# Performance work log

Hardware: AMD Instinct MI355X
Metric: run time of the kernel (lower is better)

Reference implementation:

```python
import jax, jax.numpy as jnp
import numpy as np

B, S, D, H = 4, 2048, 1024, 16
HD = D // H  # head dim = 64
EPS = 1e-12


def setup_inputs() -> dict:
    key = jax.random.key(0)
    ks = jax.random.split(key, 9)
    sc = 1.0 / np.sqrt(D)
    return {
        "X": jax.random.normal(ks[0], (B, S, D), jnp.float32),
        "Wq": jax.random.normal(ks[1], (D, D), jnp.float32) * sc,
        "bq": jnp.zeros((D,), jnp.float32),
        "Wk": jax.random.normal(ks[2], (D, D), jnp.float32) * sc,
        "bk": jnp.zeros((D,), jnp.float32),
        "Wv": jax.random.normal(ks[3], (D, D), jnp.float32) * sc,
        "bv": jnp.zeros((D,), jnp.float32),
        "Wo": jax.random.normal(ks[4], (D, D), jnp.float32) * sc,
        "bo": jnp.zeros((D,), jnp.float32),
        "gamma": jnp.ones((D,), jnp.float32),
        "beta": jnp.zeros((D,), jnp.float32),
    }


def _attention_block(X, Wq, bq, Wk, bk, Wv, bv, Wo, bo, gamma, beta):
    def heads(t):  # [B,S,D] -> [B,H,S,HD]
        return t.reshape(B, S, H, HD).transpose(0, 2, 1, 3)

    Q = heads(X @ Wq.T + bq)
    K = heads(X @ Wk.T + bk)
    V = heads(X @ Wv.T + bv)
    A = jnp.einsum("bhqd,bhkd->bhqk", Q, K) / np.sqrt(HD)
    A = jax.nn.softmax(A, axis=-1)
    O = jnp.einsum("bhqk,bhkd->bhqd", A, V)
    O = O.transpose(0, 2, 1, 3).reshape(B, S, D)
    O = O @ Wo.T + bo
    Y = O + X
    mu = Y.mean(-1, keepdims=True)
    var = jnp.square(Y - mu).mean(-1, keepdims=True)
    return gamma * (Y - mu) / jnp.sqrt(var + EPS) + beta


def reference(X, Wq, bq, Wk, bk, Wv, bv, Wo, bo, gamma, beta):
    return _attention_block(X, Wq, bq, Wk, bk, Wv, bv, Wo, bo, gamma, beta)
```

## Files before the change

### kernel.cpp

```cpp
#include <hip/hip_runtime.h>
#include <hip/hip_bf16.h>

#define B_ 4
#define S_ 2048
#define D_ 1024
#define H_ 16
#define HD_ 64
#define M_ (B_*S_)
#define BH_ (B_*H_)

typedef __bf16 bf16;
typedef __attribute__((ext_vector_type(8))) __bf16 bf16x8;
typedef __attribute__((ext_vector_type(4))) __bf16 bf16x4;
typedef __attribute__((ext_vector_type(4))) float f32x4;

#define MFMA16(a,b,c) __builtin_amdgcn_mfma_f32_16x16x32_bf16((a),(b),(c),0,0,0)

__device__ __forceinline__ void gl2lds16(const void* g, void* l) {
  __builtin_amdgcn_global_load_lds(
      (__attribute__((address_space(1))) void*)(g),
      (__attribute__((address_space(3))) void*)(l), 16, 0, 0);
}

__device__ __forceinline__ float fexp2(float x) {
  float r;
  asm("v_exp_f32 %0, %1" : "=v"(r) : "v"(x));
  return r;
}

__global__ __launch_bounds__(256) void k_cvt(const float* __restrict__ in,
                                             bf16* __restrict__ out, int n) {
  int i = (blockIdx.x * 256 + threadIdx.x) * 4;
  if (i >= n) return;
  f32x4 v = *(const f32x4*)(in + i);
  bf16x4 o;
  o[0] = (bf16)v[0]; o[1] = (bf16)v[1]; o[2] = (bf16)v[2]; o[3] = (bf16)v[3];
  *(bf16x4*)(out + i) = o;
}

template <int EPI>
__global__ __launch_bounds__(512, 4) void k_gemm(const bf16* __restrict__ A,
                                                 const bf16* __restrict__ W,
                                                 const float* __restrict__ bias,
                                                 const float* __restrict__ Xres,
                                                 void* __restrict__ outp,
                                                 float scale) {
  __shared__ __align__(16) bf16 As[2][128 * 64];
  __shared__ __align__(16) bf16 Bs[2][128 * 64];
  const int t = threadIdx.x;
  const int l = t & 63, w = t >> 6;
  const int g = l >> 4, c = l & 15;
  const int wm = w >> 2, wn = w & 3;
  const int m0 = blockIdx.y * 128, n0 = blockIdx.x * 128;

  f32x4 acc[4][2];
#pragma unroll
  for (int i = 0; i < 4; ++i)
#pragma unroll
    for (int j = 0; j < 2; ++j) acc[i][j] = (f32x4)(0.0f);

  const int srow = t >> 3;
  const int schk = t & 7;

#define STG(buf, k0)                                                          \
  do {                                                                        \
    for (int p = 0; p < 2; ++p) {                                             \
      const int row = p * 64 + srow;                                          \
      const int sc = (schk ^ (row & 7)) * 8;                                  \
      gl2lds16(A + (size_t)(m0 + row) * D_ + (k0) + sc,                       \
               &As[buf][p * 4096 + t * 8]);                                   \
      gl2lds16(W + (size_t)(n0 + row) * D_ + (k0) + sc,                       \
               &Bs[buf][p * 4096 + t * 8]);                                   \
    }                                                                         \
  } while (0)

  STG(0, 0);
  __syncthreads();

  for (int kt = 0; kt < D_ / 64; ++kt) {
    const int cur = kt & 1;
    if (kt + 1 < D_ / 64) STG(cur ^ 1, (kt + 1) * 64);
#pragma unroll
    for (int kk = 0; kk < 2; ++kk) {
      bf16x8 af[4], bw[2];
#pragma unroll
      for (int i = 0; i < 4; ++i) {
        const int ra = wm * 64 + i * 16 + c;
        af[i] = *(const bf16x8*)&As[cur][ra * 64 + (((kk * 4 + g) ^ (ra & 7)) * 8)];
      }
#pragma unroll
      for (int j = 0; j < 2; ++j) {
        const int rb = wn * 32 + j * 16 + c;
        bw[j] = *(const bf16x8*)&Bs[cur][rb * 64 + (((kk * 4 + g) ^ (rb & 7)) * 8)];
      }
#pragma unroll
      for (int i = 0; i < 4; ++i)
#pragma unroll
        for (int j = 0; j < 2; ++j) acc[i][j] = MFMA16(af[i], bw[j], acc[i][j]);
    }
    __syncthreads();
  }
#undef STG

  float bv[2];
#pragma unroll
  for (int j = 0; j < 2; ++j) bv[j] = bias[n0 + wn * 32 + j * 16 + c];

#pragma unroll
  for (int i = 0; i < 4; ++i) {
#pragma unroll
    for (int j = 0; j < 2; ++j) {
#pragma unroll
      for (int r = 0; r < 4; ++r) {
        const int m = m0 + wm * 64 + i * 16 + g * 4 + r;
        const int n = n0 + wn * 32 + j * 16 + c;
        const float v = (acc[i][j][r] + bv[j]) * scale;
        if (EPI == 2) {
          ((float*)outp)[(size_t)m * D_ + n] = v + Xres[(size_t)m * D_ + n];
        } else {
          const int b = m >> 11, s = m & (S_ - 1);
          const int h = n >> 6, hd = n & 63;
          size_t idx;
          if (EPI == 0) idx = (((size_t)(b * H_ + h)) * S_ + s) * HD_ + hd;
          else          idx = (((size_t)(b * H_ + h)) * HD_ + hd) * S_ + s;
          ((bf16*)outp)[idx] = (bf16)v;
        }
      }
    }
  }
}

__global__ __launch_bounds__(512, 4) void k_attn(const bf16* __restrict__ Q,
                                                 const bf16* __restrict__ K,
                                                 const bf16* __restrict__ Vt,
                                                 bf16* __restrict__ O) {
  __shared__ __align__(16) bf16 Ks[2][64 * 64];
  __shared__ __align__(16) bf16 Vs[2][64 * 64];
  __shared__ __align__(16) bf16 Pl[8][16 * 72];
  const int t = threadIdx.x;
  const int l = t & 63, w = t >> 6;
  const int g = l >> 4, c = l & 15;
  const int bh = blockIdx.y;
  const int q0 = blockIdx.x * 256 + w * 32;
  const bf16* Qh = Q + (size_t)bh * S_ * HD_;
  const bf16* Kh = K + (size_t)bh * S_ * HD_;
  const bf16* Vh = Vt + (size_t)bh * HD_ * S_;

  bf16x8 qf[2][2];
#pragma unroll
  for (int mf = 0; mf < 2; ++mf)
#pragma unroll
    for (int kk = 0; kk < 2; ++kk)
      qf[mf][kk] = *(const bf16x8*)&Qh[(size_t)(q0 + mf * 16 + c) * HD_ + kk * 32 + g * 8];

  f32x4 acc[2][4];
  float m_c[2], l_c[2];
#pragma unroll
  for (int mf = 0; mf < 2; ++mf) {
#pragma unroll
    for (int nf = 0; nf < 4; ++nf) acc[mf][nf] = (f32x4)(0.0f);
    m_c[mf] = -__builtin_inff();
    l_c[mf] = 0.f;
  }

  const int srow = t >> 3, schk = t & 7;

#define STGA(buf, kt)                                                         \
  do {                                                                        \
    const int sck = (schk ^ (srow & 7)) * 8;                                  \
    gl2lds16(Kh + (size_t)((kt) * 64 + srow) * HD_ + sck, &Ks[buf][t * 8]);   \
    gl2lds16(Vh + (size_t)srow * S_ + (kt) * 64 + sck, &Vs[buf][t * 8]);      \
  } while (0)

  STGA(0, 0);
  __syncthreads();

  for (int kt = 0; kt < S_ / 64; ++kt) {
    const int cur = kt & 1;
    if (kt + 1 < S_ / 64) STGA(cur ^ 1, kt + 1);

    f32x4 st[2][4];
#pragma unroll
    for (int mf = 0; mf < 2; ++mf)
#pragma unroll
      for (int nf = 0; nf < 4; ++nf) st[mf][nf] = (f32x4)(0.0f);

#pragma unroll
    for (int kk = 0; kk < 2; ++kk) {
      bf16x8 kf[4];
#pragma unroll
      for (int nf = 0; nf < 4; ++nf) {
        const int rw = nf * 16 + c;
        kf[nf] = *(const bf16x8*)&Ks[cur][rw * 64 + (((kk * 4 + g) ^ (rw & 7)) * 8)];
      }
#pragma unroll
      for (int mf = 0; mf < 2; ++mf)
#pragma unroll
        for (int nf = 0; nf < 4; ++nf)
          st[mf][nf] = MFMA16(kf[nf], qf[mf][kk], st[mf][nf]);
    }

#pragma unroll
    for (int mf = 0; mf < 2; ++mf) {
      float tm = st[mf][0][0];
#pragma unroll
      for (int nf = 0; nf < 4; ++nf)
#pragma unroll
        for (int r = 0; r < 4; ++r)
          if (nf || r) tm = fmaxf(tm, st[mf][nf][r]);
      tm = fmaxf(tm, __shfl_xor(tm, 16));
      tm = fmaxf(tm, __shfl_xor(tm, 32));
      const float mn = fmaxf(m_c[mf], tm);
      const float cfq = fexp2(m_c[mf] - mn);
      m_c[mf] = mn;
      float rs = 0.f;
#pragma unroll
      for (int nf = 0; nf < 4; ++nf) {
        bf16x4 pv;
#pragma unroll
        for (int r = 0; r < 4; ++r) {
          const float p = fexp2(st[mf][nf][r] - mn);
          rs += p;
          pv[r] = (bf16)p;
        }
        *(bf16x4*)&Pl[w][c * 72 + nf * 16 + 4 * g] = pv;
      }
      rs += __shfl_xor(rs, 16);
      rs += __shfl_xor(rs, 32);
      l_c[mf] = l_c[mf] * cfq + rs;

      float cfr[4];
#pragma unroll
      for (int r = 0; r < 4; ++r) cfr[r] = __shfl(cfq, 4 * g + r);
#pragma unroll
      for (int nf = 0; nf < 4; ++nf)
#pragma unroll
        for (int r = 0; r < 4; ++r) acc[mf][nf][r] *= cfr[r];

#pragma unroll
      for (int kk = 0; kk < 2; ++kk) {
        bf16x8 pa = *(const bf16x8*)&Pl[w][c * 72 + kk * 32 + g * 8];
        bf16x8 vf[4];
#pragma unroll
        for (int nf = 0; nf < 4; ++nf) {
          const int rw = nf * 16 + c;
          vf[nf] = *(const bf16x8*)&Vs[cur][rw * 64 + (((kk * 4 + g) ^ (rw & 7)) * 8)];
        }
#pragma unroll
        for (int nf = 0; nf < 4; ++nf)
          acc[mf][nf] = MFMA16(pa, vf[nf], acc[mf][nf]);
      }
    }
    __syncthreads();
  }
#undef STGA

  const int b = bh >> 4, h = bh & 15;
#pragma unroll
  for (int mf = 0; mf < 2; ++mf) {
    float li[4];
#pragma unroll
    for (int r = 0; r < 4; ++r)
      li[r] = __builtin_amdgcn_rcpf(__shfl(l_c[mf], 4 * g + r));
#pragma unroll
    for (int nf = 0; nf < 4; ++nf)
#pragma unroll
      for (int r = 0; r < 4; ++r) {
        const int q = q0 + mf * 16 + 4 * g + r;
        const int dv = nf * 16 + c;
        O[((size_t)(b * S_ + q)) * D_ + h * 64 + dv] = (bf16)(acc[mf][nf][r] * li[r]);
      }
  }
}

__global__ __launch_bounds__(256) void k_ln(const float* __restrict__ Y,
                                            const float* __restrict__ gamma,
                                            const float* __restrict__ beta,
                                            float* __restrict__ out) {
  __shared__ float red[8];
  const int row = blockIdx.x, t = threadIdx.x;
  const float* y = Y + (size_t)row * D_;
  f32x4 v = *(const f32x4*)(y + t * 4);
  float s = v[0] + v[1] + v[2] + v[3];
  float s2 = v[0]*v[0] + v[1]*v[1] + v[2]*v[2] + v[3]*v[3];
#pragma unroll
  for (int mk = 1; mk <= 32; mk <<= 1) {
    s += __shfl_xor(s, mk);
    s2 += __shfl_xor(s2, mk);
  }
  if ((t & 63) == 0) { red[t >> 6] = s; red[4 + (t >> 6)] = s2; }
  __syncthreads();
  const float ts = red[0] + red[1] + red[2] + red[3];
  const float ts2 = red[4] + red[5] + red[6] + red[7];
  const float mu = ts * (1.0f / D_);
  const float inv = rsqrtf(ts2 * (1.0f / D_) - mu * mu + 1e-12f);
  f32x4 gm = *(const f32x4*)(gamma + t * 4);
  f32x4 bt = *(const f32x4*)(beta + t * 4);
  f32x4 o;
#pragma unroll
  for (int j = 0; j < 4; ++j) o[j] = gm[j] * (v[j] - mu) * inv + bt[j];
  *(f32x4*)(out + (size_t)row * D_ + t * 4) = o;
}

extern "C" void kernel_launch(void* const* d_in, const int* in_sizes, int n_in,
                              void* d_out, int out_size, void* d_ws, size_t ws_size,
                              hipStream_t stream) {
  const float* X     = (const float*)d_in[0];
  const float* Wq    = (const float*)d_in[1];
  const float* bq    = (const float*)d_in[2];
  const float* Wk    = (const float*)d_in[3];
  const float* bk    = (const float*)d_in[4];
  const float* Wv    = (const float*)d_in[5];
  const float* bv    = (const float*)d_in[6];
  const float* Wo    = (const float*)d_in[7];
  const float* bo    = (const float*)d_in[8];
  const float* gamma = (const float*)d_in[9];
  const float* beta  = (const float*)d_in[10];

  char* ws = (char*)d_ws;
  bf16* Xb  = (bf16*)(ws + 0);
  bf16* Wqb = (bf16*)(ws + (16u << 20));
  bf16* Wkb = (bf16*)(ws + (18u << 20));
  bf16* Wvb = (bf16*)(ws + (20u << 20));
  bf16* Wob = (bf16*)(ws + (22u << 20));
  bf16* Qb  = (bf16*)(ws + (24u << 20));
  bf16* Kb  = (bf16*)(ws + (40u << 20));
  bf16* Vt  = (bf16*)(ws + (56u << 20));
  bf16* Ob  = (bf16*)(ws + (72u << 20));
  float* Yb = (float*)(ws + (88u << 20));

  const float SCL = 0.125f * 1.44269504088896340736f;

  k_cvt<<<M_ * D_ / 1024, 256, 0, stream>>>(X, Xb, M_ * D_);
  k_cvt<<<D_ * D_ / 1024, 256, 0, stream>>>(Wq, Wqb, D_ * D_);
  k_cvt<<<D_ * D_ / 1024, 256, 0, stream>>>(Wk, Wkb, D_ * D_);
  k_cvt<<<D_ * D_ / 1024, 256, 0, stream>>>(Wv, Wvb, D_ * D_);
  k_cvt<<<D_ * D_ / 1024, 256, 0, stream>>>(Wo, Wob, D_ * D_);

  dim3 gg(D_ / 128, M_ / 128);
  k_gemm<0><<<gg, 512, 0, stream>>>(Xb, Wqb, bq, nullptr, Qb, SCL);
  k_gemm<0><<<gg, 512, 0, stream>>>(Xb, Wkb, bk, nullptr, Kb, 1.0f);
  k_gemm<1><<<gg, 512, 0, stream>>>(Xb, Wvb, bv, nullptr, Vt, 1.0f);
  k_attn<<<dim3(S_ / 256, BH_), 512, 0, stream>>>(Qb, Kb, Vt, Ob);
  k_gemm<2><<<gg, 512, 0, stream>>>(Ob, Wob, bo, X, Yb, 1.0f);
  k_ln<<<M_, 256, 0, stream>>>(Yb, gamma, beta, (float*)d_out);
}
```

Before: 335.2 us.

## Rewrite attention inner loop with 32x32 MFMA and register-resident P

```diff
diff --git a/kernel.cpp b/kernel.cpp
--- a/kernel.cpp
+++ b/kernel.cpp
@@ -13,8 +13,11 @@
 typedef __attribute__((ext_vector_type(8))) __bf16 bf16x8;
 typedef __attribute__((ext_vector_type(4))) __bf16 bf16x4;
 typedef __attribute__((ext_vector_type(4))) float f32x4;
+typedef __attribute__((ext_vector_type(16))) float f32x16;
+typedef __attribute__((ext_vector_type(4))) unsigned u32x4;
 
 #define MFMA16(a,b,c) __builtin_amdgcn_mfma_f32_16x16x32_bf16((a),(b),(c),0,0,0)
+#define MFMA32(a,b,c) __builtin_amdgcn_mfma_f32_32x32x16_bf16((a),(b),(c),0,0,0)
 
 __device__ __forceinline__ void gl2lds16(const void* g, void* l) {
   __builtin_amdgcn_global_load_lds(
@@ -25,6 +28,12 @@
 __device__ __forceinline__ float fexp2(float x) {
   float r;
   asm("v_exp_f32 %0, %1" : "=v"(r) : "v"(x));
+  return r;
+}
+
+__device__ __forceinline__ unsigned cvtpk(float lo, float hi) {
+  unsigned r;
+  asm("v_cvt_pk_bf16_f32 %0, %1, %2" : "=v"(r) : "v"(lo), "v"(hi));
   return r;
 }
 
@@ -130,46 +139,42 @@
   }
 }
 
-__global__ __launch_bounds__(512, 4) void k_attn(const bf16* __restrict__ Q,
+__global__ __launch_bounds__(256, 3) void k_attn(const bf16* __restrict__ Q,
                                                  const bf16* __restrict__ K,
                                                  const bf16* __restrict__ Vt,
                                                  bf16* __restrict__ O) {
   __shared__ __align__(16) bf16 Ks[2][64 * 64];
   __shared__ __align__(16) bf16 Vs[2][64 * 64];
-  __shared__ __align__(16) bf16 Pl[8][16 * 72];
   const int t = threadIdx.x;
   const int l = t & 63, w = t >> 6;
-  const int g = l >> 4, c = l & 15;
+  const int c32 = l & 31, hi = l >> 5;
   const int bh = blockIdx.y;
-  const int q0 = blockIdx.x * 256 + w * 32;
+  const int q0 = blockIdx.x * 128 + w * 32;
   const bf16* Qh = Q + (size_t)bh * S_ * HD_;
   const bf16* Kh = K + (size_t)bh * S_ * HD_;
   const bf16* Vh = Vt + (size_t)bh * HD_ * S_;
 
-  bf16x8 qf[2][2];
-#pragma unroll
-  for (int mf = 0; mf < 2; ++mf)
-#pragma unroll
-    for (int kk = 0; kk < 2; ++kk)
-      qf[mf][kk] = *(const bf16x8*)&Qh[(size_t)(q0 + mf * 16 + c) * HD_ + kk * 32 + g * 8];
-
-  f32x4 acc[2][4];
-  float m_c[2], l_c[2];
-#pragma unroll
-  for (int mf = 0; mf < 2; ++mf) {
-#pragma unroll
-    for (int nf = 0; nf < 4; ++nf) acc[mf][nf] = (f32x4)(0.0f);
-    m_c[mf] = -__builtin_inff();
-    l_c[mf] = 0.f;
-  }
+  bf16x8 qf[4];
+#pragma unroll
+  for (int kk = 0; kk < 4; ++kk)
+    qf[kk] = *(const bf16x8*)&Qh[(size_t)(q0 + c32) * HD_ + kk * 16 + hi * 8];
+
+  f32x16 acc0 = (f32x16)(0.f), acc1 = (f32x16)(0.f);
+  float m_c = -__builtin_inff(), l_c = 0.f;
 
   const int srow = t >> 3, schk = t & 7;
+  const int sw = c32 & 7;
 
 #define STGA(buf, kt)                                                         \
   do {                                                                        \
-    const int sck = (schk ^ (srow & 7)) * 8;                                  \
-    gl2lds16(Kh + (size_t)((kt) * 64 + srow) * HD_ + sck, &Ks[buf][t * 8]);   \
-    gl2lds16(Vh + (size_t)srow * S_ + (kt) * 64 + sck, &Vs[buf][t * 8]);      \
+    for (int p = 0; p < 2; ++p) {                                             \
+      const int row = p * 32 + srow;                                          \
+      const int sc = (schk ^ (row & 7)) * 8;                                  \
+      gl2lds16(Kh + (size_t)((kt) * 64 + row) * HD_ + sc,                     \
+               &Ks[buf][p * 2048 + t * 8]);                                   \
+      gl2lds16(Vh + (size_t)row * S_ + (kt) * 64 + sc,                        \
+               &Vs[buf][p * 2048 + t * 8]);                                   \
+    }                                                                         \
   } while (0)
 
   STGA(0, 0);
@@ -179,97 +184,97 @@
     const int cur = kt & 1;
     if (kt + 1 < S_ / 64) STGA(cur ^ 1, kt + 1);
 
-    f32x4 st[2][4];
-#pragma unroll
-    for (int mf = 0; mf < 2; ++mf)
-#pragma unroll
-      for (int nf = 0; nf < 4; ++nf) st[mf][nf] = (f32x4)(0.0f);
-
-#pragma unroll
-    for (int kk = 0; kk < 2; ++kk) {
-      bf16x8 kf[4];
-#pragma unroll
-      for (int nf = 0; nf < 4; ++nf) {
-        const int rw = nf * 16 + c;
-        kf[nf] = *(const bf16x8*)&Ks[cur][rw * 64 + (((kk * 4 + g) ^ (rw & 7)) * 8)];
-      }
-#pragma unroll
-      for (int mf = 0; mf < 2; ++mf)
-#pragma unroll
-        for (int nf = 0; nf < 4; ++nf)
-          st[mf][nf] = MFMA16(kf[nf], qf[mf][kk], st[mf][nf]);
-    }
-
-#pragma unroll
-    for (int mf = 0; mf < 2; ++mf) {
-      float tm = st[mf][0][0];
-#pragma unroll
-      for (int nf = 0; nf < 4; ++nf)
-#pragma unroll
-        for (int r = 0; r < 4; ++r)
-          if (nf || r) tm = fmaxf(tm, st[mf][nf][r]);
-      tm = fmaxf(tm, __shfl_xor(tm, 16));
+    f32x16 st0 = (f32x16)(0.f), st1 = (f32x16)(0.f);
+    __builtin_amdgcn_s_setprio(1);
+#pragma unroll
+    for (int kk = 0; kk < 4; ++kk) {
+      const int slot = ((kk * 2 + hi) ^ sw) * 8;
+      bf16x8 kf0 = *(const bf16x8*)&Ks[cur][c32 * 64 + slot];
+      bf16x8 kf1 = *(const bf16x8*)&Ks[cur][(32 + c32) * 64 + slot];
+      st0 = MFMA32(kf0, qf[kk], st0);
+      st1 = MFMA32(kf1, qf[kk], st1);
+    }
+    __builtin_amdgcn_s_setprio(0);
+
+    float tm;
+    {
+      f32x16 mx;
+#pragma unroll
+      for (int r = 0; r < 16; ++r) mx[r] = fmaxf(st0[r], st1[r]);
+      float m8[8];
+#pragma unroll
+      for (int r = 0; r < 8; ++r) m8[r] = fmaxf(mx[r], mx[r + 8]);
+      float m4[4];
+#pragma unroll
+      for (int r = 0; r < 4; ++r) m4[r] = fmaxf(m8[r], m8[r + 4]);
+      tm = fmaxf(fmaxf(m4[0], m4[1]), fmaxf(m4[2], m4[3]));
       tm = fmaxf(tm, __shfl_xor(tm, 32));
-      const float mn = fmaxf(m_c[mf], tm);
-      const float cfq = fexp2(m_c[mf] - mn);
-      m_c[mf] = mn;
-      float rs = 0.f;
-#pragma unroll
-      for (int nf = 0; nf < 4; ++nf) {
-        bf16x4 pv;
-#pragma unroll
-        for (int r = 0; r < 4; ++r) {
-          const float p = fexp2(st[mf][nf][r] - mn);
-          rs += p;
-          pv[r] = (bf16)p;
-        }
-        *(bf16x4*)&Pl[w][c * 72 + nf * 16 + 4 * g] = pv;
-      }
-      rs += __shfl_xor(rs, 16);
-      rs += __shfl_xor(rs, 32);
-      l_c[mf] = l_c[mf] * cfq + rs;
-
-      float cfr[4];
-#pragma unroll
-      for (int r = 0; r < 4; ++r) cfr[r] = __shfl(cfq, 4 * g + r);
-#pragma unroll
-      for (int nf = 0; nf < 4; ++nf)
-#pragma unroll
-        for (int r = 0; r < 4; ++r) acc[mf][nf][r] *= cfr[r];
-
-#pragma unroll
-      for (int kk = 0; kk < 2; ++kk) {
-        bf16x8 pa = *(const bf16x8*)&Pl[w][c * 72 + kk * 32 + g * 8];
-        bf16x8 vf[4];
-#pragma unroll
-        for (int nf = 0; nf < 4; ++nf) {
-          const int rw = nf * 16 + c;
-          vf[nf] = *(const bf16x8*)&Vs[cur][rw * 64 + (((kk * 4 + g) ^ (rw & 7)) * 8)];
-        }
-#pragma unroll
-        for (int nf = 0; nf < 4; ++nf)
-          acc[mf][nf] = MFMA16(pa, vf[nf], acc[mf][nf]);
-      }
-    }
+    }
+    if (!__all(tm <= m_c + 8.f)) {
+      const float mn = fmaxf(m_c, tm);
+      const float cf = fexp2(m_c - mn);
+      m_c = mn;
+      l_c *= cf;
+#pragma unroll
+      for (int r = 0; r < 16; ++r) { acc0[r] *= cf; acc1[r] *= cf; }
+    }
+    float rs = 0.f;
+#pragma unroll
+    for (int r = 0; r < 16; ++r) { st0[r] = fexp2(st0[r] - m_c); rs += st0[r]; }
+#pragma unroll
+    for (int r = 0; r < 16; ++r) { st1[r] = fexp2(st1[r] - m_c); rs += st1[r]; }
+    rs += __shfl_xor(rs, 32);
+    l_c += rs;
+
+    unsigned ca[8], cb[8];
+#pragma unroll
+    for (int i = 0; i < 8; ++i) {
+      ca[i] = cvtpk(st0[2 * i], st0[2 * i + 1]);
+      cb[i] = cvtpk(st1[2 * i], st1[2 * i + 1]);
+    }
+    asm volatile("v_permlane32_swap_b32 %0, %1" : "+v"(ca[0]), "+v"(ca[2]));
+    asm volatile("v_permlane32_swap_b32 %0, %1" : "+v"(ca[1]), "+v"(ca[3]));
+    asm volatile("v_permlane32_swap_b32 %0, %1" : "+v"(ca[4]), "+v"(ca[6]));
+    asm volatile("v_permlane32_swap_b32 %0, %1" : "+v"(ca[5]), "+v"(ca[7]));
+    asm volatile("v_permlane32_swap_b32 %0, %1" : "+v"(cb[0]), "+v"(cb[2]));
+    asm volatile("v_permlane32_swap_b32 %0, %1" : "+v"(cb[1]), "+v"(cb[3]));
+    asm volatile("v_permlane32_swap_b32 %0, %1" : "+v"(cb[4]), "+v"(cb[6]));
+    asm volatile("v_permlane32_swap_b32 %0, %1" : "+v"(cb[5]), "+v"(cb[7]));
+    bf16x8 pf[4];
+    pf[0] = __builtin_bit_cast(bf16x8, (u32x4){ca[0], ca[1], ca[2], ca[3]});
+    pf[1] = __builtin_bit_cast(bf16x8, (u32x4){ca[4], ca[5], ca[6], ca[7]});
+    pf[2] = __builtin_bit_cast(bf16x8, (u32x4){cb[0], cb[1], cb[2], cb[3]});
+    pf[3] = __builtin_bit_cast(bf16x8, (u32x4){cb[4], cb[5], cb[6], cb[7]});
+
+    __builtin_amdgcn_s_setprio(1);
+#pragma unroll
+    for (int kb = 0; kb < 4; ++kb) {
+      const int slot = ((kb * 2 + hi) ^ sw) * 8;
+      bf16x8 vf0 = *(const bf16x8*)&Vs[cur][c32 * 64 + slot];
+      bf16x8 vf1 = *(const bf16x8*)&Vs[cur][(32 + c32) * 64 + slot];
+      acc0 = MFMA32(vf0, pf[kb], acc0);
+      acc1 = MFMA32(vf1, pf[kb], acc1);
+    }
+    __builtin_amdgcn_s_setprio(0);
+
     __syncthreads();
   }
 #undef STGA
 
+  const float li = 1.f / l_c;
   const int b = bh >> 4, h = bh & 15;
-#pragma unroll
-  for (int mf = 0; mf < 2; ++mf) {
-    float li[4];
-#pragma unroll
-    for (int r = 0; r < 4; ++r)
-      li[r] = __builtin_amdgcn_rcpf(__shfl(l_c[mf], 4 * g + r));
-#pragma unroll
-    for (int nf = 0; nf < 4; ++nf)
-#pragma unroll
-      for (int r = 0; r < 4; ++r) {
-        const int q = q0 + mf * 16 + 4 * g + r;
-        const int dv = nf * 16 + c;
-        O[((size_t)(b * S_ + q)) * D_ + h * 64 + dv] = (bf16)(acc[mf][nf][r] * li[r]);
-      }
+  const int q = q0 + c32;
+  bf16* Orow = O + ((size_t)(b * S_ + q)) * D_ + h * 64;
+#pragma unroll
+  for (int rq = 0; rq < 4; ++rq) {
+    bf16x4 o0, o1;
+#pragma unroll
+    for (int j = 0; j < 4; ++j) {
+      o0[j] = (bf16)(acc0[rq * 4 + j] * li);
+      o1[j] = (bf16)(acc1[rq * 4 + j] * li);
+    }
+    *(bf16x4*)&Orow[rq * 8 + hi * 4] = o0;
+    *(bf16x4*)&Orow[32 + rq * 8 + hi * 4] = o1;
   }
 }
 
@@ -341,7 +346,7 @@
   k_gemm<0><<<gg, 512, 0, stream>>>(Xb, Wqb, bq, nullptr, Qb, SCL);
   k_gemm<0><<<gg, 512, 0, stream>>>(Xb, Wkb, bk, nullptr, Kb, 1.0f);
   k_gemm<1><<<gg, 512, 0, stream>>>(Xb, Wvb, bv, nullptr, Vt, 1.0f);
-  k_attn<<<dim3(S_ / 256, BH_), 512, 0, stream>>>(Qb, Kb, Vt, Ob);
+  k_attn<<<dim3(S_ / 128, BH_), 256, 0, stream>>>(Qb, Kb, Vt, Ob);
   k_gemm<2><<<gg, 512, 0, stream>>>(Ob, Wob, bo, X, Yb, 1.0f);
   k_ln<<<M_, 256, 0, stream>>>(Yb, gamma, beta, (float*)d_out);
 }
```

After: 329.9 us. No clear change (-1.6%).
